# Performance work log

Hardware: AMD Instinct MI355X
Metric: run time of the kernel (lower is better)

The kernel has to match this reference:

```python
import jax, jax.numpy as jnp
import numpy as np

NUM_HEADS = 16


def setup_inputs() -> dict:
    key = jax.random.key(0)
    k1, k2, k3 = jax.random.split(key, 3)
    B, N, C = 2, 2048, 1024
    x = jax.random.normal(k1, (B, N, C), dtype=jnp.float32)
    w_qkv = jax.random.normal(k2, (3 * C, C), dtype=jnp.float32) * (C ** -0.5)
    w_proj = jax.random.normal(k3, (C, C), dtype=jnp.float32) * (C ** -0.5)
    b_proj = jnp.zeros((C,), dtype=jnp.float32)
    return {"x": x, "w_qkv": w_qkv, "w_proj": w_proj, "b_proj": b_proj}


def reference(x, w_qkv, w_proj, b_proj):
    B, N, C = x.shape
    H = NUM_HEADS
    D = C // H
    scale = 1.0 / jnp.sqrt(jnp.asarray(D, x.dtype))
    qkv = (x @ w_qkv.T).reshape(B, N, 3, H, D)
    qkv = jnp.transpose(qkv, (2, 0, 3, 1, 4))  # [3,B,H,N,D]
    q, k, v = qkv[0], qkv[1], qkv[2]
    # scaled dot-product attention with explicit score matrix [B,H,N,N]
    attn = jnp.einsum('bhnd,bhmd->bhnm', q, k) * scale
    attn = jax.nn.softmax(attn, axis=-1)
    out = jnp.einsum('bhnm,bhmd->bhnd', attn, v)
    out = jnp.transpose(out, (0, 2, 1, 3)).reshape(B, N, C)
    # output projection
    return out @ w_proj.T + b_proj
```

## Files before the change

### kernel.cpp

```cpp
#include <hip/hip_runtime.h>

typedef unsigned short u16;
typedef __attribute__((ext_vector_type(8))) short bf16x8;
typedef __attribute__((ext_vector_type(4))) float f32x4;
typedef __attribute__((ext_vector_type(16))) float f32x16;
typedef __attribute__((ext_vector_type(4))) unsigned u32x4;

#define B_ 2
#define N_ 2048
#define C_ 1024
#define H_ 16
#define D_ 64
#define M_ (B_ * N_)

#define QSCALE 0.18033688011114336f

#define EXP2R(x) __builtin_amdgcn_exp2f(x)

__device__ __forceinline__ u16 f2bf(float f) {
    union { float f; unsigned u; } x; x.f = f;
    return (u16)((x.u + 0x8000u) >> 16);
}
__device__ __forceinline__ unsigned pack2bf(float a, float b) {
    union { float f; unsigned u; } x, y; x.f = a; y.f = b;
    return __builtin_amdgcn_perm(y.u + 0x8000u, x.u + 0x8000u, 0x07060302);
}
__device__ __forceinline__ unsigned cvtpk2bf(float a, float b) {
    unsigned r;
    asm("v_cvt_pk_bf16_f32 %0, %1, %2" : "=v"(r) : "v"(a), "v"(b));
    return r;
}

__device__ __forceinline__ void async_copy16(const void* gsrc, void* ldst) {
    __builtin_amdgcn_global_load_lds(
        (__attribute__((address_space(1))) void*)gsrc,
        (__attribute__((address_space(3))) void*)ldst,
        16, 0, 0);
}

__global__ void cast3_kernel(const float* __restrict__ x, const float* __restrict__ wq,
                             const float* __restrict__ wp, u16* __restrict__ xo,
                             u16* __restrict__ wqo, u16* __restrict__ wpo) {
    int b = blockIdx.x;
    const float* s; u16* d;
    if (b < 4096)      { s = x;  d = xo;  }
    else if (b < 7168) { s = wq; d = wqo; b -= 4096; }
    else               { s = wp; d = wpo; b -= 7168; }
    int i = (b * 256 + threadIdx.x) * 4;
    const float4 v = *(const float4*)(s + i);
    uint2 o;
    o.x = pack2bf(v.x, v.y);
    o.y = pack2bf(v.z, v.w);
    *(uint2*)(d + i) = o;
}

__global__ __launch_bounds__(512, 2) void gemm_qkv8(
    const u16* __restrict__ A, const u16* __restrict__ Bm,
    u16* __restrict__ qo, u16* __restrict__ ko, u16* __restrict__ vt) {
    __shared__ u16 L[2][4][8192];
    const int tid = threadIdx.x, lane = tid & 63, w = tid >> 6;
    const int wm = w >> 2, wn = w & 3;
    const int q16 = lane >> 4, l15 = lane & 15, l7 = lane & 7;
    const int lr3 = lane >> 3, lc7 = lane & 7;
    const int sbid = (blockIdx.x & 7) * 24 + (blockIdx.x >> 3);
    const int bx = sbid % 12, by = sbid / 12;
    const int m0 = by * 256, n0 = bx * 256;
    const int cswz8 = (lc7 ^ lr3) * 8;

    auto stageHT = [&](int t, int isB, int h) {
        if (t > 15) return;
        const u16* src = isB ? Bm : A;
        int base_row = (isB ? n0 : m0) + h * 128;
#pragma unroll
        for (int i = 0; i < 2; ++i) {
            int c = w * 2 + i;
            async_copy16(src + (size_t)(base_row + c * 8 + lr3) * 1024 + t * 64 + cswz8,
                         (char*)L + ((t & 1) * 4 + isB * 2 + h) * 16384 + c * 1024);
        }
    };

    stageHT(0, 0, 0); stageHT(0, 1, 0); stageHT(0, 1, 1); stageHT(0, 0, 1);
    stageHT(1, 0, 0); stageHT(1, 1, 0); stageHT(1, 1, 1);
    asm volatile("s_waitcnt vmcnt(6)" ::: "memory");
    __builtin_amdgcn_s_barrier();

    f32x4 acc[8][4] = {};
    const int aRow = l15 * 64;
    const int colsw0 = (q16 ^ l7) * 8, colsw1 = ((4 + q16) ^ l7) * 8;
    const u16* LA[2] = { &L[0][wm][0], &L[1][wm][0] };
    const u16* LB[2] = { &L[0][2 + (wn >> 1)][0], &L[1][2 + (wn >> 1)][0] };
    const int bOff = (wn & 1) * 4096;

    bf16x8 Af[4][2], Bf0[2][2], Bf1[2][2];

    auto readA = [&](int P, int mh) {
#pragma unroll
        for (int i = 0; i < 4; ++i) {
            Af[i][0] = *(const bf16x8*)(LA[P] + (mh * 64 + i * 16) * 64 + aRow + colsw0);
            Af[i][1] = *(const bf16x8*)(LA[P] + (mh * 64 + i * 16) * 64 + aRow + colsw1);
        }
    };
    auto readB = [&](int P, int nh, bf16x8 (*Bf)[2]) {
#pragma unroll
        for (int j = 0; j < 2; ++j) {
            Bf[j][0] = *(const bf16x8*)(LB[P] + bOff + (nh * 32 + j * 16) * 64 + aRow + colsw0);
            Bf[j][1] = *(const bf16x8*)(LB[P] + bOff + (nh * 32 + j * 16) * 64 + aRow + colsw1);
        }
    };
    auto mfma16 = [&](int mh, int nh, bf16x8 (*Bf)[2]) {
        __builtin_amdgcn_s_setprio(1);
#pragma unroll
        for (int i = 0; i < 4; ++i)
#pragma unroll
            for (int j = 0; j < 2; ++j)
#pragma unroll
                for (int ks = 0; ks < 2; ++ks)
                    acc[mh * 4 + i][nh * 2 + j] = __builtin_amdgcn_mfma_f32_16x16x32_bf16(
                        Af[i][ks], Bf[j][ks], acc[mh * 4 + i][nh * 2 + j], 0, 0, 0);
        __builtin_amdgcn_s_setprio(0);
    };

    for (int it = 0; it < 8; ++it) {
        const int T = 2 * it;
        readA(0, 0); readB(0, 0, Bf0); stageHT(T + 1, 0, 1);
        __builtin_amdgcn_s_barrier();
        mfma16(0, 0, Bf0);
        __builtin_amdgcn_s_barrier();
        readB(0, 1, Bf1);
        __builtin_amdgcn_s_barrier();
        mfma16(0, 1, Bf1);
        __builtin_amdgcn_s_barrier();
        readA(0, 1); stageHT(T + 2, 1, 0);
        __builtin_amdgcn_s_barrier();
        mfma16(1, 1, Bf1);
        __builtin_amdgcn_s_barrier();
        stageHT(T + 2, 1, 1); stageHT(T + 2, 0, 0);
        __builtin_amdgcn_s_barrier();
        mfma16(1, 0, Bf0);
        if (it < 7) { asm volatile("s_waitcnt vmcnt(6)" ::: "memory"); }
        else        { asm volatile("s_waitcnt vmcnt(0)" ::: "memory"); }
        __builtin_amdgcn_s_barrier();
        readA(1, 0); readB(1, 0, Bf0); stageHT(T + 2, 0, 1);
        __builtin_amdgcn_s_barrier();
        mfma16(0, 0, Bf0);
        __builtin_amdgcn_s_barrier();
        readB(1, 1, Bf1);
        __builtin_amdgcn_s_barrier();
        mfma16(0, 1, Bf1);
        __builtin_amdgcn_s_barrier();
        readA(1, 1); stageHT(T + 3, 1, 0);
        __builtin_amdgcn_s_barrier();
        mfma16(1, 1, Bf1);
        __builtin_amdgcn_s_barrier();
        stageHT(T + 3, 1, 1); stageHT(T + 3, 0, 0);
        __builtin_amdgcn_s_barrier();
        mfma16(1, 0, Bf0);
        if (it < 7) { asm volatile("s_waitcnt vmcnt(6)" ::: "memory"); }
        __builtin_amdgcn_s_barrier();
    }

#pragma unroll
    for (int fm = 0; fm < 8; ++fm) {
#pragma unroll
        for (int fn = 0; fn < 4; ++fn) {
            int n_g = n0 + wn * 64 + fn * 16 + l15;
            int which = n_g >> 10;
            int h = (n_g >> 6) & 15;
            int d = n_g & 63;
            int m_base = m0 + wm * 128 + fm * 16 + q16 * 4;
            int b = m_base >> 11;
            int nn0 = m_base & 2047;
            if (which == 2) {
                uint2 pk;
                pk.x = pack2bf(acc[fm][fn][0], acc[fm][fn][1]);
                pk.y = pack2bf(acc[fm][fn][2], acc[fm][fn][3]);
                *(uint2*)(vt + ((size_t)((b * H_ + h) * D_ + d) << 11) + nn0) = pk;
            } else {
                size_t base = ((size_t)((b * H_ + h) * N_ + nn0) << 6) + d;
#pragma unroll
                for (int r = 0; r < 4; ++r) {
                    float v = acc[fm][fn][r];
                    if (which == 0) qo[base + (size_t)r * D_] = f2bf(v * QSCALE);
                    else            ko[base + (size_t)r * D_] = f2bf(v);
                }
            }
        }
    }
}

__global__ __launch_bounds__(256, 4) void gemm_out(
    const u16* __restrict__ A, const u16* __restrict__ Bm,
    const float* __restrict__ bias, float* __restrict__ out) {
    __shared__ u16 As[64 * 64];
    __shared__ u16 Bs[64 * 64];
    const int K = C_, Ncols = C_, ntiles_n = 16;
    const int tid = threadIdx.x, lane = tid & 63, w = tid >> 6;
    const int cpx = gridDim.x >> 3;
    const int sbid = (blockIdx.x & 7) * cpx + (blockIdx.x >> 3);
    const int bx = sbid % ntiles_n, by = sbid / ntiles_n;
    const int m0 = by * 64, n0 = bx * 64;
    const int wm = w >> 1, wn = w & 1;
    const int q16 = lane >> 4, l15 = lane & 15;
    const int r0 = lane >> 3, c0 = (lane & 7) * 8;
    f32x4 acc[2][2] = {};

    for (int k0 = 0; k0 < K; k0 += 64) {
#pragma unroll
        for (int i = 0; i < 2; ++i) {
            int blk = w * 2 + i;
            int r = blk * 8 + r0;
            async_copy16(A + (size_t)(m0 + r) * K + k0 + c0, (char*)As + blk * 1024);
            async_copy16(Bm + (size_t)(n0 + r) * K + k0 + c0, (char*)Bs + blk * 1024);
        }
        __builtin_amdgcn_s_waitcnt(0);
        __syncthreads();
#pragma unroll
        for (int ks = 0; ks < 2; ++ks) {
            bf16x8 af[2], bf[2];
#pragma unroll
            for (int i = 0; i < 2; ++i) {
                af[i] = *(const bf16x8*)&As[(wm * 32 + i * 16 + l15) * 64 + ks * 32 + q16 * 8];
                bf[i] = *(const bf16x8*)&Bs[(wn * 32 + i * 16 + l15) * 64 + ks * 32 + q16 * 8];
            }
            __builtin_amdgcn_s_setprio(1);
#pragma unroll
            for (int mi = 0; mi < 2; ++mi)
#pragma unroll
                for (int ni = 0; ni < 2; ++ni)
                    acc[mi][ni] = __builtin_amdgcn_mfma_f32_16x16x32_bf16(af[mi], bf[ni], acc[mi][ni], 0, 0, 0);
            __builtin_amdgcn_s_setprio(0);
        }
        __syncthreads();
    }

#pragma unroll
    for (int mi = 0; mi < 2; ++mi) {
#pragma unroll
        for (int ni = 0; ni < 2; ++ni) {
            int n_g = n0 + wn * 32 + ni * 16 + l15;
#pragma unroll
            for (int r = 0; r < 4; ++r) {
                int m_g = m0 + wm * 32 + mi * 16 + q16 * 4 + r;
                out[(size_t)m_g * Ncols + n_g] = acc[mi][ni][r] + bias[n_g];
            }
        }
    }
}

__global__ __launch_bounds__(512, 1) void attn_kernel(
    const u16* __restrict__ Q, const u16* __restrict__ K,
    const u16* __restrict__ VT, u16* __restrict__ O) {
    __shared__ u16 Ks[2][2][64 * 64];
    __shared__ u16 Vs[2][2][64 * 64];
    const int tid = threadIdx.x, lane = tid & 63, w = tid >> 6;
    const int l31 = lane & 31, hi = lane >> 5;
    const int bid = blockIdx.x;
    const int bh = (bid & 7) * 4 + (bid >> 6);
    const int q0 = ((bid >> 3) & 7) * 256;
    const size_t head = (size_t)bh * N_ * D_;

    auto stage = [&](int kt, int buf) {
        int key0 = kt * 128;
#pragma unroll
        for (int s = 0; s < 2; ++s) {
            async_copy16(K + head + (size_t)(key0 + s * 64 + lane) * D_ + w * 8,
                         (char*)Ks[buf][s] + w * 1024);
            async_copy16(VT + head + (size_t)lane * N_ + key0 + s * 64 + w * 8,
                         (char*)Vs[buf][s] + w * 1024);
        }
    };

    bf16x8 qf[4];
#pragma unroll
    for (int ds = 0; ds < 4; ++ds)
        qf[ds] = *(const bf16x8*)(Q + head + (size_t)(q0 + w * 32 + l31) * D_ + ds * 16 + hi * 8);
    stage(0, 0);
    __builtin_amdgcn_s_waitcnt(0);
    __syncthreads();

    f32x16 o_acc[2] = {};
    float rs = 0.f;

    for (int kt = 0; kt < 16; ++kt) {
        int buf = kt & 1;
        stage((kt + 1) & 15, buf ^ 1);

#pragma unroll
        for (int s = 0; s < 2; ++s) {
#pragma unroll
            for (int kb2 = 0; kb2 < 2; ++kb2) {
                f32x16 st = {};
                __builtin_amdgcn_s_setprio(1);
#pragma unroll
                for (int ds = 0; ds < 4; ++ds) {
                    bf16x8 kf = *(const bf16x8*)&Ks[buf][s][(ds * 2 + hi) * 512 + (kb2 * 32 + l31) * 8];
                    st = __builtin_amdgcn_mfma_f32_32x32x16_bf16(kf, qf[ds], st, 0, 0, 0);
                }
                __builtin_amdgcn_s_setprio(0);

                float p[16];
#pragma unroll
                for (int i = 0; i < 16; ++i) p[i] = EXP2R(st[i]);
#pragma unroll
                for (int i = 0; i < 16; ++i) rs += p[i];

                unsigned a0 = cvtpk2bf(p[0], p[1]),   b0 = cvtpk2bf(p[4], p[5]);
                unsigned a1 = cvtpk2bf(p[2], p[3]),   b1 = cvtpk2bf(p[6], p[7]);
                unsigned a2 = cvtpk2bf(p[8], p[9]),   b2 = cvtpk2bf(p[12], p[13]);
                unsigned a3 = cvtpk2bf(p[10], p[11]), b3 = cvtpk2bf(p[14], p[15]);
                asm("v_permlane32_swap_b32 %0, %1" : "+v"(a0), "+v"(b0));
                asm("v_permlane32_swap_b32 %0, %1" : "+v"(a1), "+v"(b1));
                asm("v_permlane32_swap_b32 %0, %1" : "+v"(a2), "+v"(b2));
                asm("v_permlane32_swap_b32 %0, %1" : "+v"(a3), "+v"(b3));
                union { u32x4 u; bf16x8 v; } af0, af1;
                af0.u = (u32x4){a0, a1, b0, b1};
                af1.u = (u32x4){a2, a3, b2, b3};

                __builtin_amdgcn_s_setprio(1);
#pragma unroll
                for (int db = 0; db < 2; ++db) {
                    bf16x8 vf0 = *(const bf16x8*)&Vs[buf][s][(kb2 * 4 + hi) * 512 + (db * 32 + l31) * 8];
                    o_acc[db] = __builtin_amdgcn_mfma_f32_32x32x16_bf16(af0.v, vf0, o_acc[db], 0, 0, 0);
                    bf16x8 vf1 = *(const bf16x8*)&Vs[buf][s][(kb2 * 4 + 2 + hi) * 512 + (db * 32 + l31) * 8];
                    o_acc[db] = __builtin_amdgcn_mfma_f32_32x32x16_bf16(af1.v, vf1, o_acc[db], 0, 0, 0);
                }
                __builtin_amdgcn_s_setprio(0);
            }
        }

        __builtin_amdgcn_s_waitcnt(0);
        __syncthreads();
    }

    rs += __shfl_xor(rs, 32);
    float rsi = 1.0f / rs;

    const int b = bh >> 4, h = bh & 15;
#pragma unroll
    for (int reg = 0; reg < 16; ++reg) {
        int qrow = (reg & 3) + 8 * (reg >> 2) + 4 * hi;
        float inv = __shfl(rsi, qrow);
        int qg = q0 + w * 32 + qrow;
#pragma unroll
        for (int db = 0; db < 2; ++db) {
            int d = db * 32 + l31;
            O[((size_t)(b * N_ + qg) << 10) + h * 64 + d] = f2bf(o_acc[db][reg] * inv);
        }
    }
}

extern "C" void kernel_launch(void* const* d_in, const int* in_sizes, int n_in,
                              void* d_out, int out_size, void* d_ws, size_t ws_size,
                              hipStream_t stream) {
    const float* x      = (const float*)d_in[0];
    const float* w_qkv  = (const float*)d_in[1];
    const float* w_proj = (const float*)d_in[2];
    const float* b_proj = (const float*)d_in[3];
    float* out = (float*)d_out;

    char* ws = (char*)d_ws;
    const size_t MB = 1024 * 1024;
    u16* x_bf     = (u16*)(ws + 0 * MB);
    u16* wqkv_bf  = (u16*)(ws + 8 * MB);
    u16* wproj_bf = (u16*)(ws + 14 * MB);
    u16* q_bf     = (u16*)(ws + 16 * MB);
    u16* k_bf     = (u16*)(ws + 24 * MB);
    u16* vt_bf    = (u16*)(ws + 32 * MB);
    u16* ao_bf    = (u16*)(ws + 40 * MB);

    cast3_kernel<<<8192, 256, 0, stream>>>(x, w_qkv, w_proj, x_bf, wqkv_bf, wproj_bf);

    gemm_qkv8<<<192, 512, 0, stream>>>(x_bf, wqkv_bf, q_bf, k_bf, vt_bf);

    attn_kernel<<<256, 512, 0, stream>>>(q_bf, k_bf, vt_bf, ao_bf);

    gemm_out<<<64 * 16, 256, 0, stream>>>(ao_bf, wproj_bf, b_proj, out);
}
```

Before: 184.7 us.

## Stage K/V through registers with coalesced loads and XOR-swizzled LDS layout

Replaces direct async global-to-LDS copies for K and V tiles with register-staged loads. Each wave now reads contiguous 128-byte rows, which coalesces better, and writes them into LDS under an XOR swizzle keyed by the 8-element group index. The MFMA fragment reads apply the matching swizzle to reduce bank conflicts. The cost is extra VGPRs to hold the prefetched tiles, plus explicit ds_write instructions at the end of each iteration where the async copies previously bypassed registers.

```diff
diff --git a/kernel.cpp b/kernel.cpp
--- a/kernel.cpp
+++ b/kernel.cpp
@@ -254,19 +254,29 @@
     __shared__ u16 Vs[2][2][64 * 64];
     const int tid = threadIdx.x, lane = tid & 63, w = tid >> 6;
     const int l31 = lane & 31, hi = lane >> 5;
+    const int lr3 = lane >> 3, lc7 = lane & 7;
     const int bid = blockIdx.x;
     const int bh = (bid & 7) * 4 + (bid >> 6);
     const int q0 = ((bid >> 3) & 7) * 256;
     const size_t head = (size_t)bh * N_ * D_;
-
-    auto stage = [&](int kt, int buf) {
+    const int row8 = w * 8 + lr3;
+    const int widx = ((row8 ^ lc7) * 8);
+
+    bf16x8 stK[2], stV[2];
+
+    auto issue = [&](int kt) {
         int key0 = kt * 128;
 #pragma unroll
         for (int s = 0; s < 2; ++s) {
-            async_copy16(K + head + (size_t)(key0 + s * 64 + lane) * D_ + w * 8,
-                         (char*)Ks[buf][s] + w * 1024);
-            async_copy16(VT + head + (size_t)lane * N_ + key0 + s * 64 + w * 8,
-                         (char*)Vs[buf][s] + w * 1024);
+            stK[s] = *(const bf16x8*)(K + head + (size_t)(key0 + s * 64 + row8) * D_ + lc7 * 8);
+            stV[s] = *(const bf16x8*)(VT + head + (size_t)row8 * N_ + key0 + s * 64 + lc7 * 8);
+        }
+    };
+    auto commit = [&](int buf) {
+#pragma unroll
+        for (int s = 0; s < 2; ++s) {
+            *(bf16x8*)&Ks[buf][s][lc7 * 512 + widx] = stK[s];
+            *(bf16x8*)&Vs[buf][s][lc7 * 512 + widx] = stV[s];
         }
     };
 
@@ -274,8 +284,8 @@
 #pragma unroll
     for (int ds = 0; ds < 4; ++ds)
         qf[ds] = *(const bf16x8*)(Q + head + (size_t)(q0 + w * 32 + l31) * D_ + ds * 16 + hi * 8);
-    stage(0, 0);
-    __builtin_amdgcn_s_waitcnt(0);
+    issue(0);
+    commit(0);
     __syncthreads();
 
     f32x16 o_acc[2] = {};
@@ -283,7 +293,7 @@
 
     for (int kt = 0; kt < 16; ++kt) {
         int buf = kt & 1;
-        stage((kt + 1) & 15, buf ^ 1);
+        issue((kt + 1) & 15);
 
 #pragma unroll
         for (int s = 0; s < 2; ++s) {
@@ -293,7 +303,8 @@
                 __builtin_amdgcn_s_setprio(1);
 #pragma unroll
                 for (int ds = 0; ds < 4; ++ds) {
-                    bf16x8 kf = *(const bf16x8*)&Ks[buf][s][(ds * 2 + hi) * 512 + (kb2 * 32 + l31) * 8];
+                    int g = ds * 2 + hi;
+                    bf16x8 kf = *(const bf16x8*)&Ks[buf][s][g * 512 + ((kb2 * 32 + l31) ^ g) * 8];
                     st = __builtin_amdgcn_mfma_f32_32x32x16_bf16(kf, qf[ds], st, 0, 0, 0);
                 }
                 __builtin_amdgcn_s_setprio(0);
@@ -319,16 +330,17 @@
                 __builtin_amdgcn_s_setprio(1);
 #pragma unroll
                 for (int db = 0; db < 2; ++db) {
-                    bf16x8 vf0 = *(const bf16x8*)&Vs[buf][s][(kb2 * 4 + hi) * 512 + (db * 32 + l31) * 8];
+                    int g0 = kb2 * 4 + hi, g1 = kb2 * 4 + 2 + hi;
+                    bf16x8 vf0 = *(const bf16x8*)&Vs[buf][s][g0 * 512 + ((db * 32 + l31) ^ g0) * 8];
                     o_acc[db] = __builtin_amdgcn_mfma_f32_32x32x16_bf16(af0.v, vf0, o_acc[db], 0, 0, 0);
-                    bf16x8 vf1 = *(const bf16x8*)&Vs[buf][s][(kb2 * 4 + 2 + hi) * 512 + (db * 32 + l31) * 8];
+                    bf16x8 vf1 = *(const bf16x8*)&Vs[buf][s][g1 * 512 + ((db * 32 + l31) ^ g1) * 8];
                     o_acc[db] = __builtin_amdgcn_mfma_f32_32x32x16_bf16(af1.v, vf1, o_acc[db], 0, 0, 0);
                 }
                 __builtin_amdgcn_s_setprio(0);
             }
         }
 
-        __builtin_amdgcn_s_waitcnt(0);
+        commit(buf ^ 1);
         __syncthreads();
     }
 
```

After: 174.3 us. 1.06x faster.
